# Kernel tuning notes

Hardware: AMD Instinct MI355X
Metric: run time of the kernel (lower is better)

Reference implementation:

```python
import jax, jax.numpy as jnp
from jax import lax
import numpy as np

B, NUM_TPM, NUM_CNV, NODE_DIM, DRUG_FEAT = 32, 16000, 16000, 36, 75
N_DRUGS, N_ATOMS, N_PAIRS = 128, 64, 4096


def setup_inputs() -> dict:
    key = jax.random.key(0)
    ks = jax.random.split(key, 32)

    def w(k, shape):
        fan_in = shape[0] if len(shape) == 2 else int(np.prod(shape[1:]))
        return (jax.random.normal(k, shape, jnp.float32) / np.float32(np.sqrt(fan_in))).astype(jnp.float32)

    pic_dim = jax.random.normal(ks[0], (B, 3, 256, 256), jnp.float32)
    rna_seq = jax.random.normal(ks[1], (B, NUM_TPM), jnp.float32)
    gene_cnv = jax.random.normal(ks[2], (B, NUM_CNV), jnp.float32)
    drug_fea = jax.random.uniform(ks[3], (N_DRUGS, N_ATOMS, DRUG_FEAT), jnp.float32)
    a = (jax.random.uniform(ks[4], (N_DRUGS, N_ATOMS, N_ATOMS)) < 0.15).astype(jnp.float32)
    drug_adj = jnp.maximum(a, jnp.transpose(a, (0, 2, 1)))
    index_list = jnp.stack([
        jax.random.randint(ks[5], (N_PAIRS,), 0, B),
        jax.random.randint(ks[6], (N_PAIRS,), 0, N_DRUGS)], axis=1)
    target = jax.random.randint(ks[7], (N_PAIRS,), 0, 2)
    logit_scale = jnp.asarray(10.0, jnp.float32)
    return dict(
        pic_dim=pic_dim, rna_seq=rna_seq, gene_cnv=gene_cnv,
        drug_fea=drug_fea, drug_adj=drug_adj, index_list=index_list,
        target=target, logit_scale=logit_scale,
        conv_w=w(ks[8], (32, 3, 5, 5)), conv_b=jnp.zeros((32,), jnp.float32),
        fc1_w=w(ks[9], (32 * 128 * 128, 1024)), fc1_b=jnp.zeros((1024,), jnp.float32),
        fc2_w=w(ks[10], (1024, 36)), fc2_b=jnp.zeros((36,), jnp.float32),
        mlp1_w1=w(ks[11], (NUM_TPM, NUM_TPM // 4)), mlp1_b1=jnp.zeros((NUM_TPM // 4,), jnp.float32),
        mlp1_w2=w(ks[12], (NUM_TPM // 4, NODE_DIM)), mlp1_b2=jnp.zeros((NODE_DIM,), jnp.float32),
        mlp2_w1=w(ks[13], (NUM_CNV, NUM_CNV // 4)), mlp2_b1=jnp.zeros((NUM_CNV // 4,), jnp.float32),
        mlp2_w2=w(ks[14], (NUM_CNV // 4, NODE_DIM)), mlp2_b2=jnp.zeros((NODE_DIM,), jnp.float32),
        att_w1=w(ks[15], (36, 128)), att_b1=jnp.zeros((128,), jnp.float32),
        att_w2=w(ks[16], (128, 1)),
        end_w1=w(ks[17], (NODE_DIM * 4, NODE_DIM)), end_b1=jnp.zeros((NODE_DIM,), jnp.float32),
        end_w2=w(ks[18], (NODE_DIM, 2)), end_b2=jnp.zeros((2,), jnp.float32),
        gcn_w=w(ks[19], (DRUG_FEAT, NODE_DIM * 8)), gcn_w2=w(ks[20], (NODE_DIM * 8, NODE_DIM * 2)))


def _mlp(x, w1, b1, w2, b2):  # Linear-ReLU-(Dropout eval)-Linear-Softmax
    h = jax.nn.relu(x @ w1 + b1)
    return jax.nn.softmax(h @ w2 + b2, axis=-1)


def _ce(logits, labels):  # mean cross entropy, labels int [N]
    lp = jax.nn.log_softmax(logits, axis=-1)
    return -jnp.take_along_axis(lp, labels[:, None], axis=1).mean()


def reference(pic_dim, rna_seq, gene_cnv, drug_fea, drug_adj, index_list, target,
              logit_scale, conv_w, conv_b, fc1_w, fc1_b, fc2_w, fc2_b,
              mlp1_w1, mlp1_b1, mlp1_w2, mlp1_b2, mlp2_w1, mlp2_b1, mlp2_w2, mlp2_b2,
              att_w1, att_b1, att_w2, end_w1, end_b1, end_w2, end_b2, gcn_w, gcn_w2):
    # omics branches
    rna1 = _mlp(rna_seq, mlp1_w1, mlp1_b1, mlp1_w2, mlp1_b2)    # [B,36]
    cnv1 = _mlp(gene_cnv, mlp2_w1, mlp2_b1, mlp2_w2, mlp2_b2)   # [B,36]
    # image branch: conv(3->32,k5,p2) + relu + maxpool2 + fc
    x = lax.conv_general_dilated(pic_dim, conv_w, (1, 1), [(2, 2), (2, 2)])
    x = jax.nn.relu(x + conv_b[None, :, None, None])
    x = lax.reduce_window(x, -jnp.inf, lax.max, (1, 1, 2, 2), (1, 1, 2, 2), 'VALID')
    x = x.reshape(x.shape[0], -1)                               # [B, 32*128*128]
    x = jax.nn.relu(x @ fc1_w + fc1_b)
    pic1 = x @ fc2_w + fc2_b                                    # [B,36]
    # semantic attention over the two omics views
    z = jnp.stack([rna1, cnv1], axis=1)                         # [B,2,36]
    wv = (jnp.tanh(z @ att_w1 + att_b1) @ att_w2).mean(0)       # [2,1]
    beta = jax.nn.softmax(wv, axis=0)
    cell = (beta[None] * z).sum(1)                              # [B,36]
    # CLIP-style loss
    pic1 = pic1 / jnp.linalg.norm(pic1, axis=1, keepdims=True)
    cell = cell / jnp.linalg.norm(cell, axis=1, keepdims=True)
    image_fea = logit_scale * (pic1 @ cell.T)
    labels = jnp.arange(image_fea.shape[0])
    total_loss2 = (_ce(image_fea, labels) + _ce(image_fea.T, labels)) / 2
    cell_cat = jnp.concatenate([cell, pic1], axis=1)            # [B,72]
    # batched drug GCN (replaces per-drug python loop)
    eye = jnp.eye(N_ATOMS, dtype=jnp.float32)
    def gcn_one(X, A):
        Ht = A.T * (1.0 - eye) + eye        # set diagonal to 1 (add self loops)
        deg = Ht.sum(1)
        dinv = jnp.where(deg == 0, 0.0, 1.0 / deg)
        Hn = dinv[:, None] * Ht             # D^-1 A_hat  (== H.t() after norm)
        out = Hn @ ((Hn @ (X @ gcn_w)) @ gcn_w2)
        return jnp.max(jax.nn.relu(out), axis=0)  # max over atoms -> [72]
    drugfea = jax.vmap(gcn_one)(drug_fea, drug_adj)             # [n_drugs,72]
    # pair prediction head
    Bc = jnp.concatenate([cell_cat[index_list[:, 0]], drugfea[index_list[:, 1]]], axis=1)
    Bp = _mlp(Bc, end_w1, end_b1, end_w2, end_b2)               # [n_pairs,2]
    loss1 = _ce(Bp, target)
    return (loss1, total_loss2, Bp, target)
```

## Files before the change

### kernel.cpp

```cpp
#include <hip/hip_runtime.h>
#include <hip/hip_bf16.h>
#include <math.h>

typedef float evf4 __attribute__((ext_vector_type(4)));

__device__ __forceinline__ void fma4(float4& a, float s, const float4& v) {
  a.x += s * v.x; a.y += s * v.y; a.z += s * v.z; a.w += s * v.w;
}
__device__ __forceinline__ float4 ntload4(const float4* p) {
  evf4 v = __builtin_nontemporal_load((const evf4*)p);
  return make_float4(v.x, v.y, v.z, v.w);
}
__device__ __forceinline__ float ntload1(const float* p) {
  return __builtin_nontemporal_load(p);
}

__device__ __forceinline__ void conv_body(
    const float* __restrict__ pic, const float* __restrict__ cw,
    const float* __restrict__ cb, float* __restrict__ pooled,
    int bid, float tile[3][8][260]) {
  int php = bid & 63, ocg2 = (bid >> 6) & 1, b = bid >> 7;
  int tid = threadIdx.x;
  int pw = tid & 127, phl = tid >> 7;
  int ph = php * 2 + phl;
  int h_base = php * 4 - 2;
  for (int i = tid; i < 3 * 8 * 260; i += 256) {
    int c = i % 260; int rr = (i / 260) & 7; int ic = i / (260 * 8);
    int h = h_base + rr, w = c - 2;
    float v = 0.f;
    if (h >= 0 && h < 256 && w >= 0 && w < 256)
      v = pic[((size_t)b * 3 + ic) * 65536 + h * 256 + w];
    tile[ic][rr][c] = v;
  }
  __syncthreads();
  float acc[16][4];
#pragma unroll
  for (int o = 0; o < 16; ++o)
#pragma unroll
    for (int q = 0; q < 4; ++q) acc[o][q] = 0.f;
  int r0 = phl * 2;
  int c0 = pw * 2;
#pragma unroll
  for (int ic = 0; ic < 3; ++ic) {
    float win[6][6];
#pragma unroll
    for (int r = 0; r < 6; ++r)
#pragma unroll
      for (int cc = 0; cc < 6; ++cc) win[r][cc] = tile[ic][r0 + r][c0 + cc];
#pragma unroll
    for (int o = 0; o < 16; ++o) {
      const float* __restrict__ wk = cw + ((ocg2 * 16 + o) * 3 + ic) * 25;
#pragma unroll
      for (int kh = 0; kh < 5; ++kh)
#pragma unroll
        for (int kw = 0; kw < 5; ++kw) {
          float wv = wk[kh * 5 + kw];
          acc[o][0] += win[kh][kw] * wv;
          acc[o][1] += win[kh][kw + 1] * wv;
          acc[o][2] += win[kh + 1][kw] * wv;
          acc[o][3] += win[kh + 1][kw + 1] * wv;
        }
    }
  }
#pragma unroll
  for (int o = 0; o < 16; ++o) {
    float m = fmaxf(fmaxf(acc[o][0], acc[o][1]), fmaxf(acc[o][2], acc[o][3]));
    m = fmaxf(m + cb[ocg2 * 16 + o], 0.f);
    pooled[(((size_t)b * 32 + ocg2 * 16 + o) * 128 + ph) * 128 + pw] = m;
  }
}

__device__ __forceinline__ void wc_body(
    const float* __restrict__ w1, const float* __restrict__ w2,
    float* __restrict__ wc, int bx) {
  int i = bx * 256 + threadIdx.x;
  if (i >= 75 * 72) return;
  int r = i / 72, c = i - r * 72;
  float s = 0.f;
  for (int k = 0; k < 288; ++k) s += w1[r * 288 + k] * w2[k * 72 + c];
  wc[i] = s;
}

__global__ __launch_bounds__(256) void k1_conv_wc_kernel(
    const float* __restrict__ pic, const float* __restrict__ cw,
    const float* __restrict__ cb, float* __restrict__ pooled,
    const float* __restrict__ gw, const float* __restrict__ gw2,
    float* __restrict__ wcb) {
  __shared__ float tile[3][8][260];
  int bid = blockIdx.x;
  if (bid < 4096) conv_body(pic, cw, cb, pooled, bid, tile);
  else            wc_body(gw, gw2, wcb, bid - 4096);
}

__device__ __forceinline__ void gemm32p_body(
    const float* __restrict__ X, const float* __restrict__ W,
    float* __restrict__ partial, int K, int N, int chunk,
    int bx, int split, float xs[128][36]) {
  int tid = threadIdx.x;
  int colv = bx * 256 + tid;
  int col0 = colv * 4;
  bool active = col0 < N;
  int k0 = split * chunk, k1 = min(k0 + chunk, K);
  size_t Nv = (size_t)(N >> 2);
  const float4* Wv = (const float4*)W;
  float4 acc[32];
#pragma unroll
  for (int b = 0; b < 32; ++b) acc[b] = make_float4(0.f, 0.f, 0.f, 0.f);

  float4 xpre[4];
#pragma unroll
  for (int j = 0; j < 4; ++j) {
    int idx = tid + j * 256;
    int b = idx >> 5, kk = (idx & 31) * 4;
    xpre[j] = *(const float4*)&X[(size_t)b * K + k0 + kk];
  }

  auto fmablk = [&](int kk, const float4& w4) {
    const float4* xr = (const float4*)xs[kk];
#pragma unroll
    for (int b4 = 0; b4 < 8; ++b4) {
      float4 xv = xr[b4];
      fma4(acc[b4 * 4 + 0], xv.x, w4);
      fma4(acc[b4 * 4 + 1], xv.y, w4);
      fma4(acc[b4 * 4 + 2], xv.z, w4);
      fma4(acc[b4 * 4 + 3], xv.w, w4);
    }
  };

  for (int kt = k0; kt < k1; kt += 128) {
    __syncthreads();
#pragma unroll
    for (int j = 0; j < 4; ++j) {
      int idx = tid + j * 256;
      int b = idx >> 5, kk = (idx & 31) * 4;
      xs[kk + 0][b] = xpre[j].x;
      xs[kk + 1][b] = xpre[j].y;
      xs[kk + 2][b] = xpre[j].z;
      xs[kk + 3][b] = xpre[j].w;
    }
    __syncthreads();
    if (kt + 128 < k1) {
#pragma unroll
      for (int j = 0; j < 4; ++j) {
        int idx = tid + j * 256;
        int b = idx >> 5, kk = (idx & 31) * 4;
        xpre[j] = *(const float4*)&X[(size_t)b * K + kt + 128 + kk];
      }
    }
    if (active) {
      const float4* wp = Wv + (size_t)kt * Nv + colv;
      float4 cur[8], nxt[8];
#pragma unroll
      for (int j = 0; j < 8; ++j) cur[j] = ntload4(wp + (size_t)j * Nv);
#pragma unroll 1
      for (int g = 0; g < 15; ++g) {
        const float4* wn = wp + 8 * Nv;
#pragma unroll
        for (int j = 0; j < 8; ++j) nxt[j] = ntload4(wn + (size_t)j * Nv);
        int kb = g * 8;
#pragma unroll
        for (int j = 0; j < 8; ++j) fmablk(kb + j, cur[j]);
#pragma unroll
        for (int j = 0; j < 8; ++j) cur[j] = nxt[j];
        wp = wn;
      }
#pragma unroll
      for (int j = 0; j < 8; ++j) fmablk(120 + j, cur[j]);
    }
  }
  if (active) {
    float* p = partial + (size_t)split * 32 * N + col0;
#pragma unroll
    for (int b = 0; b < 32; ++b) *(float4*)(p + (size_t)b * N) = acc[b];
  }
}

__global__ __launch_bounds__(256) void gemm_all_kernel(
    const float* __restrict__ pooled, const float* __restrict__ fc1w,
    float* __restrict__ pfc1,
    const float* __restrict__ rna, const float* __restrict__ m1w1, float* __restrict__ pm1,
    const float* __restrict__ cnv, const float* __restrict__ m2w1, float* __restrict__ pm2) {
  __shared__ float xs[128][36];
  int b = blockIdx.x;
  if (b < 512) {
    gemm32p_body(pooled, fc1w, pfc1, 524288, 1024, 1024, 0, b, xs);
  } else {
    int j = b - 512;
    int z = j / 252;
    int r = j % 252;
    int bx = r & 3, split = r >> 2;
    if (z == 0) gemm32p_body(rna, m1w1, pm1, 16000, 4000, 256, bx, split, xs);
    else        gemm32p_body(cnv, m2w1, pm2, 16000, 4000, 256, bx, split, xs);
  }
}

__device__ __forceinline__ void reduce_s1_body(
    const float* __restrict__ partial, float* __restrict__ p2, int N,
    int bx, int sy) {
  int i = bx * 256 + threadIdx.x;
  if (i >= 32 * N) return;
  const float* p = partial + (size_t)(sy * 128) * 32 * N + i;
  size_t st = (size_t)32 * N;
  float s0 = 0, s1 = 0, s2 = 0, s3 = 0, s4 = 0, s5 = 0, s6 = 0, s7 = 0;
  for (int sp = 0; sp < 128; sp += 8) {
    s0 += ntload1(p + (sp + 0) * st); s1 += ntload1(p + (sp + 1) * st);
    s2 += ntload1(p + (sp + 2) * st); s3 += ntload1(p + (sp + 3) * st);
    s4 += ntload1(p + (sp + 4) * st); s5 += ntload1(p + (sp + 5) * st);
    s6 += ntload1(p + (sp + 6) * st); s7 += ntload1(p + (sp + 7) * st);
  }
  p2[(size_t)sy * 32 * N + i] = ((s0 + s1) + (s2 + s3)) + ((s4 + s5) + (s6 + s7));
}

__device__ __forceinline__ void reduce8_body(
    const float* __restrict__ partial, const float* __restrict__ bias,
    float* __restrict__ out, int N, int nsplit, int relu, int bx) {
  int i = bx * 256 + threadIdx.x;
  if (i >= 32 * N) return;
  int col = i % N;
  const float* p = partial + i;
  size_t st = (size_t)32 * N;
  float s0 = 0, s1 = 0, s2 = 0, s3 = 0, s4 = 0, s5 = 0, s6 = 0, s7 = 0;
  int sp = 0;
  for (; sp + 8 <= nsplit; sp += 8) {
    s0 += ntload1(p + (sp + 0) * st); s1 += ntload1(p + (sp + 1) * st);
    s2 += ntload1(p + (sp + 2) * st); s3 += ntload1(p + (sp + 3) * st);
    s4 += ntload1(p + (sp + 4) * st); s5 += ntload1(p + (sp + 5) * st);
    s6 += ntload1(p + (sp + 6) * st); s7 += ntload1(p + (sp + 7) * st);
  }
  for (; sp < nsplit; ++sp) s0 += ntload1(p + (size_t)sp * st);
  float s = bias[col] + (((s0 + s1) + (s2 + s3)) + ((s4 + s5) + (s6 + s7)));
  out[i] = relu ? fmaxf(s, 0.f) : s;
}

__global__ __launch_bounds__(256) void k3_reduce_kernel(
    const float* __restrict__ pfc1, float* __restrict__ p2fc1,
    const float* __restrict__ pm1, const float* __restrict__ m1b1, float* __restrict__ h1,
    const float* __restrict__ pm2, const float* __restrict__ m2b1, float* __restrict__ h2) {
  int b = blockIdx.x;
  if (b < 512) {
    reduce_s1_body(pfc1, p2fc1, 1024, b & 127, b >> 7);
  } else {
    int idx = b - 512;
    if (idx < 500) reduce8_body(pm1, m1b1, h1, 4000, 63, 1, idx);
    else           reduce8_body(pm2, m2b1, h2, 4000, 63, 1, idx - 500);
  }
}

__device__ __forceinline__ void reduce_s2_body(
    const float* __restrict__ p2, const float* __restrict__ bias,
    float* __restrict__ out, int N, int nsy, int relu, int bx) {
  int i = bx * 256 + threadIdx.x;
  if (i >= 32 * N) return;
  int col = i % N;
  float s = bias[col];
  for (int sy = 0; sy < nsy; ++sy) s += p2[(size_t)sy * 32 * N + i];
  out[i] = relu ? fmaxf(s, 0.f) : s;
}

__device__ __forceinline__ void gcn_body(
    const float* __restrict__ Xg, const float* __restrict__ Ag,
    const float* __restrict__ Wc, float* __restrict__ drugfea, int d,
    float Hn[64][65], float Xs[64][75], float Wcs[75][72],
    float Ys[64][72], float Ts[64][72]) {
  int tid = threadIdx.x;
  const float* Ad = Ag + (size_t)d * 4096;
  const float* Xd = Xg + (size_t)d * 4800;
  for (int i = tid; i < 4096; i += 256) {
    int r = i & 63, c = i >> 6;
    Hn[r][c] = (r == c) ? 1.f : Ad[c * 64 + r];
  }
  for (int i = tid; i < 4800; i += 256) Xs[i / 75][i % 75] = Xd[i];
  for (int i = tid; i < 5400; i += 256) Wcs[i / 72][i % 72] = Wc[i];
  __syncthreads();
  if (tid < 64) {
    float s = 0.f;
    for (int c = 0; c < 64; ++c) s += Hn[tid][c];
    float inv = (s == 0.f) ? 0.f : 1.f / s;
    for (int c = 0; c < 64; ++c) Hn[tid][c] *= inv;
  }
  __syncthreads();
  int rb = tid >> 3, cb = tid & 7;
  int r0 = rb * 2, c0 = cb * 9;
  {
    float o0[9], o1[9];
#pragma unroll
    for (int j = 0; j < 9; ++j) { o0[j] = 0.f; o1[j] = 0.f; }
    for (int k = 0; k < 75; ++k) {
      float x0 = Xs[r0][k], x1 = Xs[r0 + 1][k];
#pragma unroll
      for (int j = 0; j < 9; ++j) {
        float w = Wcs[k][c0 + j];
        o0[j] += x0 * w; o1[j] += x1 * w;
      }
    }
#pragma unroll
    for (int j = 0; j < 9; ++j) { Ys[r0][c0 + j] = o0[j]; Ys[r0 + 1][c0 + j] = o1[j]; }
  }
  __syncthreads();
  {
    float o0[9], o1[9];
#pragma unroll
    for (int j = 0; j < 9; ++j) { o0[j] = 0.f; o1[j] = 0.f; }
    for (int k = 0; k < 64; ++k) {
      float x0 = Hn[r0][k], x1 = Hn[r0 + 1][k];
#pragma unroll
      for (int j = 0; j < 9; ++j) {
        float w = Ys[k][c0 + j];
        o0[j] += x0 * w; o1[j] += x1 * w;
      }
    }
#pragma unroll
    for (int j = 0; j < 9; ++j) { Ts[r0][c0 + j] = o0[j]; Ts[r0 + 1][c0 + j] = o1[j]; }
  }
  __syncthreads();
  {
    float o0[9], o1[9];
#pragma unroll
    for (int j = 0; j < 9; ++j) { o0[j] = 0.f; o1[j] = 0.f; }
    for (int k = 0; k < 64; ++k) {
      float x0 = Hn[r0][k], x1 = Hn[r0 + 1][k];
#pragma unroll
      for (int j = 0; j < 9; ++j) {
        float w = Ts[k][c0 + j];
        o0[j] += x0 * w; o1[j] += x1 * w;
      }
    }
#pragma unroll
    for (int j = 0; j < 9; ++j) {
      Ys[r0][c0 + j] = fmaxf(o0[j], 0.f);
      Ys[r0 + 1][c0 + j] = fmaxf(o1[j], 0.f);
    }
  }
  __syncthreads();
  if (tid < 72) {
    float m = Ys[0][tid];
    for (int i = 1; i < 64; ++i) m = fmaxf(m, Ys[i][tid]);
    drugfea[d * 72 + tid] = m;
  }
}

__global__ __launch_bounds__(256) void k4_s2_gcn_kernel(
    const float* __restrict__ p2fc1, const float* __restrict__ fc1_b,
    float* __restrict__ fcact,
    const float* __restrict__ Xg, const float* __restrict__ Ag,
    const float* __restrict__ wcb, float* __restrict__ drugfea) {
  __shared__ float Hn[64][65];
  __shared__ float Xs[64][75];
  __shared__ float Wcs[75][72];
  __shared__ float Ys[64][72];
  __shared__ float Ts[64][72];
  int b = blockIdx.x;
  if (b < 128) reduce_s2_body(p2fc1, fc1_b, fcact, 1024, 4, 1, b);
  else         gcn_body(Xg, Ag, wcb, drugfea, b - 128, Hn, Xs, Wcs, Ys, Ts);
}

__global__ __launch_bounds__(256) void lin36_all_kernel(
    const float* __restrict__ X0, const float* __restrict__ W0,
    const float* __restrict__ bi0, float* __restrict__ out0,
    const float* __restrict__ X1, const float* __restrict__ W1,
    const float* __restrict__ bi1, float* __restrict__ out1,
    const float* __restrict__ X2, const float* __restrict__ W2,
    const float* __restrict__ bi2, float* __restrict__ out2) {
  const float* X; const float* W; const float* bias; float* out; int K; bool do_sm;
  if (blockIdx.y == 0)      { X = X0; W = W0; bias = bi0; out = out0; K = 4000; do_sm = true; }
  else if (blockIdx.y == 1) { X = X1; W = W1; bias = bi1; out = out1; K = 4000; do_sm = true; }
  else                      { X = X2; W = W2; bias = bi2; out = out2; K = 1024; do_sm = false; }
  __shared__ float xs[4000];
  __shared__ float red[28][36];
  __shared__ float vals[36];
  __shared__ float mxv, smv;
  int b = blockIdx.x, tid = threadIdx.x;
  for (int i = tid; i < K; i += 256) xs[i] = X[(size_t)b * K + i];
  __syncthreads();
  if (tid < 252) {
    int c4 = tid % 9, g = tid / 9;
    const float4* W4 = (const float4*)W;
    float4 s = make_float4(0.f, 0.f, 0.f, 0.f);
    for (int k = g; k < K; k += 28) fma4(s, xs[k], W4[k * 9 + c4]);
    red[g][c4 * 4 + 0] = s.x; red[g][c4 * 4 + 1] = s.y;
    red[g][c4 * 4 + 2] = s.z; red[g][c4 * 4 + 3] = s.w;
  }
  __syncthreads();
  if (tid < 36) {
    float s = bias[tid];
    for (int g = 0; g < 28; ++g) s += red[g][tid];
    vals[tid] = s;
  }
  __syncthreads();
  if (do_sm) {
    if (tid == 0) {
      float m = -1e30f;
      for (int j = 0; j < 36; ++j) m = fmaxf(m, vals[j]);
      float e = 0.f;
      for (int j = 0; j < 36; ++j) e += expf(vals[j] - m);
      mxv = m; smv = e;
    }
    __syncthreads();
    if (tid < 36) out[b * 36 + tid] = expf(vals[tid] - mxv) / smv;
  } else {
    if (tid < 36) out[b * 36 + tid] = vals[tid];
  }
}

__global__ __launch_bounds__(256) void head_kernel(
    const float* __restrict__ rna1, const float* __restrict__ cnv1,
    const float* __restrict__ pic1r, const float* __restrict__ aw1,
    const float* __restrict__ ab1, const float* __restrict__ aw2,
    const float* __restrict__ scale_p, float* __restrict__ cell_cat,
    float* __restrict__ dout) {
  __shared__ float z[2][32][36];
  __shared__ float pic1n[32][36];
  __shared__ float celln[32][36];
  __shared__ float fea[32][32];
  __shared__ float wvp[64];
  __shared__ float beta0, beta1;
  __shared__ float rowl[32], coll[32];
  int tid = threadIdx.x;
  for (int i = tid; i < 1152; i += 256) {
    int b = i / 36, k = i - (i / 36) * 36;
    z[0][b][k] = rna1[i];
    z[1][b][k] = cnv1[i];
    pic1n[b][k] = pic1r[i];
  }
  __syncthreads();
  {
    int p = tid >> 2, sub = tid & 3;
    int b = p >> 1, v = p & 1;
    float s = 0.f;
    for (int h = sub; h < 128; h += 4) {
      float a = ab1[h];
      for (int k = 0; k < 36; ++k) a += z[v][b][k] * aw1[k * 128 + h];
      s += tanhf(a) * aw2[h];
    }
    s += __shfl_down(s, 1, 64);
    s += __shfl_down(s, 2, 64);
    if (sub == 0) wvp[p] = s;
  }
  __syncthreads();
  if (tid == 0) {
    float w0 = 0.f, w1 = 0.f;
    for (int b = 0; b < 32; ++b) { w0 += wvp[b * 2]; w1 += wvp[b * 2 + 1]; }
    w0 /= 32.f; w1 /= 32.f;
    float m = fmaxf(w0, w1);
    float e0 = expf(w0 - m), e1 = expf(w1 - m);
    beta0 = e0 / (e0 + e1); beta1 = e1 / (e0 + e1);
  }
  __syncthreads();
  for (int i = tid; i < 1152; i += 256) {
    int b = i / 36, k = i - (i / 36) * 36;
    celln[b][k] = beta0 * z[0][b][k] + beta1 * z[1][b][k];
  }
  __syncthreads();
  if (tid < 32) {
    float s = 0.f;
    for (int k = 0; k < 36; ++k) { float x = pic1n[tid][k]; s += x * x; }
    float inv = 1.f / sqrtf(s);
    for (int k = 0; k < 36; ++k) pic1n[tid][k] *= inv;
  } else if (tid < 64) {
    int b = tid - 32;
    float s = 0.f;
    for (int k = 0; k < 36; ++k) { float x = celln[b][k]; s += x * x; }
    float inv = 1.f / sqrtf(s);
    for (int k = 0; k < 36; ++k) celln[b][k] *= inv;
  }
  __syncthreads();
  for (int i = tid; i < 1152; i += 256) {
    int b = i / 36, k = i - (i / 36) * 36;
    cell_cat[b * 72 + k] = celln[b][k];
    cell_cat[b * 72 + 36 + k] = pic1n[b][k];
  }
  float sc = *scale_p;
  for (int t = tid; t < 1024; t += 256) {
    int i = t >> 5, j = t & 31;
    float s = 0.f;
    for (int k = 0; k < 36; ++k) s += pic1n[i][k] * celln[j][k];
    fea[i][j] = sc * s;
  }
  __syncthreads();
  if (tid < 32) {
    float m = -1e30f;
    for (int j = 0; j < 32; ++j) m = fmaxf(m, fea[tid][j]);
    float e = 0.f;
    for (int j = 0; j < 32; ++j) e += expf(fea[tid][j] - m);
    rowl[tid] = (logf(e) + m) - fea[tid][tid];
  } else if (tid < 64) {
    int j = tid - 32;
    float m = -1e30f;
    for (int i = 0; i < 32; ++i) m = fmaxf(m, fea[i][j]);
    float e = 0.f;
    for (int i = 0; i < 32; ++i) e += expf(fea[i][j] - m);
    coll[j] = (logf(e) + m) - fea[j][j];
  }
  __syncthreads();
  if (tid == 0) {
    float s1 = 0.f, s2 = 0.f;
    for (int i = 0; i < 32; ++i) { s1 += rowl[i]; s2 += coll[i]; }
    dout[1] = 0.5f * (s1 / 32.f + s2 / 32.f);
  }
}

__global__ __launch_bounds__(256) void pair_kernel(
    const float* __restrict__ cell_cat, const float* __restrict__ drugfea,
    const int* __restrict__ idx, const int* __restrict__ target,
    const float* __restrict__ w1, const float* __restrict__ b1,
    const float* __restrict__ w2, const float* __restrict__ b2,
    float* __restrict__ bp_out, float* __restrict__ tgt_out,
    float* __restrict__ blocksums) {
  __shared__ float w1s[144][36];
  __shared__ float ccs[32][73];
  __shared__ float dfs[128][73];
  __shared__ float w2s[72], b2s[2];
  __shared__ float lsum[256];
  int tid = threadIdx.x;
  {
    float4* dst = (float4*)&w1s[0][0];
    const float4* src = (const float4*)w1;
    for (int i = tid; i < 1296; i += 256) dst[i] = src[i];
  }
  for (int i = tid; i < 2304; i += 256) ccs[i / 72][i % 72] = cell_cat[i];
  for (int i = tid; i < 9216; i += 256) dfs[i / 72][i % 72] = drugfea[i];
  if (tid < 72) w2s[tid] = w2[tid];
  if (tid < 2) b2s[tid] = b2[tid];
  __syncthreads();
  int p = blockIdx.x * 256 + tid;
  int ci = idx[p * 2], dj = idx[p * 2 + 1];
  float4 h4[9];
  {
    const float4* bb = (const float4*)b1;
#pragma unroll
    for (int q = 0; q < 9; ++q) h4[q] = bb[q];
  }
  for (int k = 0; k < 72; ++k) {
    float x = ccs[ci][k];
    const float4* wr = (const float4*)&w1s[k][0];
#pragma unroll
    for (int q = 0; q < 9; ++q) fma4(h4[q], x, wr[q]);
  }
  for (int k = 0; k < 72; ++k) {
    float x = dfs[dj][k];
    const float4* wr = (const float4*)&w1s[72 + k][0];
#pragma unroll
    for (int q = 0; q < 9; ++q) fma4(h4[q], x, wr[q]);
  }
  float l0 = b2s[0], l1 = b2s[1];
#pragma unroll
  for (int q = 0; q < 9; ++q) {
    float hv;
    hv = fmaxf(h4[q].x, 0.f); l0 += hv * w2s[(q * 4 + 0) * 2]; l1 += hv * w2s[(q * 4 + 0) * 2 + 1];
    hv = fmaxf(h4[q].y, 0.f); l0 += hv * w2s[(q * 4 + 1) * 2]; l1 += hv * w2s[(q * 4 + 1) * 2 + 1];
    hv = fmaxf(h4[q].z, 0.f); l0 += hv * w2s[(q * 4 + 2) * 2]; l1 += hv * w2s[(q * 4 + 2) * 2 + 1];
    hv = fmaxf(h4[q].w, 0.f); l0 += hv * w2s[(q * 4 + 3) * 2]; l1 += hv * w2s[(q * 4 + 3) * 2 + 1];
  }
  float m = fmaxf(l0, l1);
  float e0 = expf(l0 - m), e1 = expf(l1 - m);
  float inv = 1.f / (e0 + e1);
  float p0 = e0 * inv, p1 = e1 * inv;
  bp_out[p * 2] = p0;
  bp_out[p * 2 + 1] = p1;
  int t = target[p];
  float mm = fmaxf(p0, p1);
  float lse = logf(expf(p0 - mm) + expf(p1 - mm)) + mm;
  float chosen = t ? p1 : p0;
  lsum[tid] = lse - chosen;
  tgt_out[p] = (float)t;
  __syncthreads();
  for (int s = 128; s > 0; s >>= 1) {
    if (tid < s) lsum[tid] += lsum[tid + s];
    __syncthreads();
  }
  if (tid == 0) blocksums[blockIdx.x] = lsum[0];
}

__global__ void final_kernel(const float* __restrict__ blocksums, float* __restrict__ dout) {
  if (threadIdx.x == 0 && blockIdx.x == 0) {
    float s = 0.f;
    for (int i = 0; i < 16; ++i) s += blocksums[i];
    dout[0] = s / 4096.f;
  }
}

extern "C" void kernel_launch(void* const* d_in, const int* in_sizes, int n_in,
                              void* d_out, int out_size, void* d_ws, size_t ws_size,
                              hipStream_t stream) {
  (void)in_sizes; (void)n_in; (void)out_size; (void)ws_size;
  const float* pic        = (const float*)d_in[0];
  const float* rna        = (const float*)d_in[1];
  const float* cnv        = (const float*)d_in[2];
  const float* drug_fea   = (const float*)d_in[3];
  const float* drug_adj   = (const float*)d_in[4];
  const int*   index_list = (const int*)d_in[5];
  const int*   target     = (const int*)d_in[6];
  const float* logit_scale= (const float*)d_in[7];
  const float* conv_w     = (const float*)d_in[8];
  const float* conv_b     = (const float*)d_in[9];
  const float* fc1_w      = (const float*)d_in[10];
  const float* fc1_b      = (const float*)d_in[11];
  const float* fc2_w      = (const float*)d_in[12];
  const float* fc2_b      = (const float*)d_in[13];
  const float* m1w1       = (const float*)d_in[14];
  const float* m1b1       = (const float*)d_in[15];
  const float* m1w2       = (const float*)d_in[16];
  const float* m1b2       = (const float*)d_in[17];
  const float* m2w1       = (const float*)d_in[18];
  const float* m2b1       = (const float*)d_in[19];
  const float* m2w2       = (const float*)d_in[20];
  const float* m2b2       = (const float*)d_in[21];
  const float* aw1        = (const float*)d_in[22];
  const float* ab1        = (const float*)d_in[23];
  const float* aw2        = (const float*)d_in[24];
  const float* ew1        = (const float*)d_in[25];
  const float* eb1        = (const float*)d_in[26];
  const float* ew2        = (const float*)d_in[27];
  const float* eb2        = (const float*)d_in[28];
  const float* gw         = (const float*)d_in[29];
  const float* gw2        = (const float*)d_in[30];

  float* ws = (float*)d_ws;
  float* pooled  = ws;
  float* pfc1    = ws + 16777216;
  float* p2fc1   = ws + 33554432;
  float* pm1     = ws + 33685504;
  float* pm2     = ws + 41749504;
  float* fcact   = ws + 49813504;
  float* h1      = ws + 49846272;
  float* h2      = ws + 49974272;
  float* rna1    = ws + 50102272;
  float* cnv1    = ws + 50103424;
  float* pic1r   = ws + 50104576;
  float* wcb     = ws + 50105728;
  float* drugf   = ws + 50111128;
  float* cellcat = ws + 50120344;
  float* bsums   = ws + 50122648;

  float* out = (float*)d_out;

  k1_conv_wc_kernel<<<4118, 256, 0, stream>>>(pic, conv_w, conv_b, pooled,
                                              gw, gw2, wcb);
  gemm_all_kernel<<<1016, 256, 0, stream>>>(pooled, fc1_w, pfc1,
                                            rna, m1w1, pm1, cnv, m2w1, pm2);
  k3_reduce_kernel<<<1512, 256, 0, stream>>>(pfc1, p2fc1,
                                             pm1, m1b1, h1, pm2, m2b1, h2);
  k4_s2_gcn_kernel<<<256, 256, 0, stream>>>(p2fc1, fc1_b, fcact,
                                            drug_fea, drug_adj, wcb, drugf);
  {
    dim3 g(32, 3);
    lin36_all_kernel<<<g, 256, 0, stream>>>(h1, m1w2, m1b2, rna1,
                                            h2, m2w2, m2b2, cnv1,
                                            fcact, fc2_w, fc2_b, pic1r);
  }
  head_kernel<<<1, 256, 0, stream>>>(rna1, cnv1, pic1r, aw1, ab1, aw2,
                                     logit_scale, cellcat, out);
  pair_kernel<<<16, 256, 0, stream>>>(cellcat, drugf, index_list, target,
                                      ew1, eb1, ew2, eb2,
                                      out + 2, out + 2 + 8192, bsums);
  final_kernel<<<1, 64, 0, stream>>>(bsums, out);
}
```

Before: 1.007 ms.

## Narrow GEMM columns per thread to two and vectorize split-K reductions

The split-K GEMM body now handles two output columns per thread instead of four. This halves the accumulator registers so the kernel can declare four blocks per SIMD, and the grid grows to cover the same work (fc1 now uses 256 splits of 2048 with two column blocks). The register prefetch of the X tile for the next step is dropped. The reduction kernels are rewritten to use float4 nontemporal loads with hardcoded sizes, so fewer blocks are launched. The trade-off is less reuse of each shared-memory X read per weight load, and the X load latency is no longer hidden behind the compute.

After: 1.993 ms. 97.9% more time.

```diff
diff --git a/kernel.cpp b/kernel.cpp
--- a/kernel.cpp
+++ b/kernel.cpp
@@ -3,6 +3,7 @@
 #include <math.h>
 
 typedef float evf4 __attribute__((ext_vector_type(4)));
+typedef float evf2 __attribute__((ext_vector_type(2)));
 
 __device__ __forceinline__ void fma4(float4& a, float s, const float4& v) {
   a.x += s * v.x; a.y += s * v.y; a.z += s * v.z; a.w += s * v.w;
@@ -11,8 +12,9 @@
   evf4 v = __builtin_nontemporal_load((const evf4*)p);
   return make_float4(v.x, v.y, v.z, v.w);
 }
-__device__ __forceinline__ float ntload1(const float* p) {
-  return __builtin_nontemporal_load(p);
+__device__ __forceinline__ float2 ntload2(const float2* p) {
+  evf2 v = __builtin_nontemporal_load((const evf2*)p);
+  return make_float2(v.x, v.y);
 }
 
 __device__ __forceinline__ void conv_body(
@@ -92,38 +94,30 @@
   else            wc_body(gw, gw2, wcb, bid - 4096);
 }
 
-__device__ __forceinline__ void gemm32p_body(
+__device__ __forceinline__ void gemm2c_body(
     const float* __restrict__ X, const float* __restrict__ W,
     float* __restrict__ partial, int K, int N, int chunk,
     int bx, int split, float xs[128][36]) {
   int tid = threadIdx.x;
   int colv = bx * 256 + tid;
-  int col0 = colv * 4;
+  int col0 = colv * 2;
   bool active = col0 < N;
   int k0 = split * chunk, k1 = min(k0 + chunk, K);
-  size_t Nv = (size_t)(N >> 2);
-  const float4* Wv = (const float4*)W;
-  float4 acc[32];
-#pragma unroll
-  for (int b = 0; b < 32; ++b) acc[b] = make_float4(0.f, 0.f, 0.f, 0.f);
-
-  float4 xpre[4];
-#pragma unroll
-  for (int j = 0; j < 4; ++j) {
-    int idx = tid + j * 256;
-    int b = idx >> 5, kk = (idx & 31) * 4;
-    xpre[j] = *(const float4*)&X[(size_t)b * K + k0 + kk];
-  }
-
-  auto fmablk = [&](int kk, const float4& w4) {
+  size_t Nv = (size_t)(N >> 1);
+  const float2* Wv = (const float2*)W;
+  float2 acc[32];
+#pragma unroll
+  for (int b = 0; b < 32; ++b) acc[b] = make_float2(0.f, 0.f);
+
+  auto fmablk = [&](int kk, const float2& w2) {
     const float4* xr = (const float4*)xs[kk];
 #pragma unroll
     for (int b4 = 0; b4 < 8; ++b4) {
       float4 xv = xr[b4];
-      fma4(acc[b4 * 4 + 0], xv.x, w4);
-      fma4(acc[b4 * 4 + 1], xv.y, w4);
-      fma4(acc[b4 * 4 + 2], xv.z, w4);
-      fma4(acc[b4 * 4 + 3], xv.w, w4);
+      acc[b4 * 4 + 0].x += xv.x * w2.x; acc[b4 * 4 + 0].y += xv.x * w2.y;
+      acc[b4 * 4 + 1].x += xv.y * w2.x; acc[b4 * 4 + 1].y += xv.y * w2.y;
+      acc[b4 * 4 + 2].x += xv.z * w2.x; acc[b4 * 4 + 2].y += xv.z * w2.y;
+      acc[b4 * 4 + 3].x += xv.w * w2.x; acc[b4 * 4 + 3].y += xv.w * w2.y;
     }
   };
 
@@ -133,30 +127,21 @@
     for (int j = 0; j < 4; ++j) {
       int idx = tid + j * 256;
       int b = idx >> 5, kk = (idx & 31) * 4;
-      xs[kk + 0][b] = xpre[j].x;
-      xs[kk + 1][b] = xpre[j].y;
-      xs[kk + 2][b] = xpre[j].z;
-      xs[kk + 3][b] = xpre[j].w;
+      float4 x = *(const float4*)&X[(size_t)b * K + kt + kk];
+      xs[kk + 0][b] = x.x; xs[kk + 1][b] = x.y;
+      xs[kk + 2][b] = x.z; xs[kk + 3][b] = x.w;
     }
     __syncthreads();
-    if (kt + 128 < k1) {
-#pragma unroll
-      for (int j = 0; j < 4; ++j) {
-        int idx = tid + j * 256;
-        int b = idx >> 5, kk = (idx & 31) * 4;
-        xpre[j] = *(const float4*)&X[(size_t)b * K + kt + 128 + kk];
-      }
-    }
     if (active) {
-      const float4* wp = Wv + (size_t)kt * Nv + colv;
-      float4 cur[8], nxt[8];
-#pragma unroll
-      for (int j = 0; j < 8; ++j) cur[j] = ntload4(wp + (size_t)j * Nv);
+      const float2* wp = Wv + (size_t)kt * Nv + colv;
+      float2 cur[8], nxt[8];
+#pragma unroll
+      for (int j = 0; j < 8; ++j) cur[j] = ntload2(wp + (size_t)j * Nv);
 #pragma unroll 1
       for (int g = 0; g < 15; ++g) {
-        const float4* wn = wp + 8 * Nv;
-#pragma unroll
-        for (int j = 0; j < 8; ++j) nxt[j] = ntload4(wn + (size_t)j * Nv);
+        const float2* wn = wp + 8 * Nv;
+#pragma unroll
+        for (int j = 0; j < 8; ++j) nxt[j] = ntload2(wn + (size_t)j * Nv);
         int kb = g * 8;
 #pragma unroll
         for (int j = 0; j < 8; ++j) fmablk(kb + j, cur[j]);
@@ -171,11 +156,11 @@
   if (active) {
     float* p = partial + (size_t)split * 32 * N + col0;
 #pragma unroll
-    for (int b = 0; b < 32; ++b) *(float4*)(p + (size_t)b * N) = acc[b];
-  }
-}
-
-__global__ __launch_bounds__(256) void gemm_all_kernel(
+    for (int b = 0; b < 32; ++b) *(float2*)(p + (size_t)b * N) = acc[b];
+  }
+}
+
+__global__ __launch_bounds__(256, 4) void gemm_all_kernel(
     const float* __restrict__ pooled, const float* __restrict__ fc1w,
     float* __restrict__ pfc1,
     const float* __restrict__ rna, const float* __restrict__ m1w1, float* __restrict__ pm1,
@@ -183,53 +168,65 @@
   __shared__ float xs[128][36];
   int b = blockIdx.x;
   if (b < 512) {
-    gemm32p_body(pooled, fc1w, pfc1, 524288, 1024, 1024, 0, b, xs);
+    gemm2c_body(pooled, fc1w, pfc1, 524288, 1024, 2048, b & 1, b >> 1, xs);
   } else {
     int j = b - 512;
-    int z = j / 252;
-    int r = j % 252;
-    int bx = r & 3, split = r >> 2;
-    if (z == 0) gemm32p_body(rna, m1w1, pm1, 16000, 4000, 256, bx, split, xs);
-    else        gemm32p_body(cnv, m2w1, pm2, 16000, 4000, 256, bx, split, xs);
-  }
+    int z = j / 504;
+    int r = j % 504;
+    int bx = r & 7, split = r >> 3;
+    if (z == 0) gemm2c_body(rna, m1w1, pm1, 16000, 4000, 256, bx, split, xs);
+    else        gemm2c_body(cnv, m2w1, pm2, 16000, 4000, 256, bx, split, xs);
+  }
+}
+
+__device__ __forceinline__ void fadd4(float4& a, const float4& v) {
+  a.x += v.x; a.y += v.y; a.z += v.z; a.w += v.w;
 }
 
 __device__ __forceinline__ void reduce_s1_body(
-    const float* __restrict__ partial, float* __restrict__ p2, int N,
+    const float* __restrict__ partial, float* __restrict__ p2,
     int bx, int sy) {
   int i = bx * 256 + threadIdx.x;
-  if (i >= 32 * N) return;
-  const float* p = partial + (size_t)(sy * 128) * 32 * N + i;
-  size_t st = (size_t)32 * N;
-  float s0 = 0, s1 = 0, s2 = 0, s3 = 0, s4 = 0, s5 = 0, s6 = 0, s7 = 0;
-  for (int sp = 0; sp < 128; sp += 8) {
-    s0 += ntload1(p + (sp + 0) * st); s1 += ntload1(p + (sp + 1) * st);
-    s2 += ntload1(p + (sp + 2) * st); s3 += ntload1(p + (sp + 3) * st);
-    s4 += ntload1(p + (sp + 4) * st); s5 += ntload1(p + (sp + 5) * st);
-    s6 += ntload1(p + (sp + 6) * st); s7 += ntload1(p + (sp + 7) * st);
-  }
-  p2[(size_t)sy * 32 * N + i] = ((s0 + s1) + (s2 + s3)) + ((s4 + s5) + (s6 + s7));
-}
-
-__device__ __forceinline__ void reduce8_body(
+  const float4* p = (const float4*)partial + (size_t)(sy * 128) * 8192 + i;
+  const size_t st = 8192;
+  float4 s0 = make_float4(0, 0, 0, 0), s1 = s0, s2 = s0, s3 = s0;
+  for (int sp = 0; sp < 128; sp += 4) {
+    fadd4(s0, ntload4(p + (sp + 0) * st));
+    fadd4(s1, ntload4(p + (sp + 1) * st));
+    fadd4(s2, ntload4(p + (sp + 2) * st));
+    fadd4(s3, ntload4(p + (sp + 3) * st));
+  }
+  float4 r;
+  r.x = (s0.x + s1.x) + (s2.x + s3.x);
+  r.y = (s0.y + s1.y) + (s2.y + s3.y);
+  r.z = (s0.z + s1.z) + (s2.z + s3.z);
+  r.w = (s0.w + s1.w) + (s2.w + s3.w);
+  ((float4*)p2)[(size_t)sy * 8192 + i] = r;
+}
+
+__device__ __forceinline__ void reduce_mlp_body(
     const float* __restrict__ partial, const float* __restrict__ bias,
-    float* __restrict__ out, int N, int nsplit, int relu, int bx) {
+    float* __restrict__ out, int bx) {
   int i = bx * 256 + threadIdx.x;
-  if (i >= 32 * N) return;
-  int col = i % N;
-  const float* p = partial + i;
-  size_t st = (size_t)32 * N;
-  float s0 = 0, s1 = 0, s2 = 0, s3 = 0, s4 = 0, s5 = 0, s6 = 0, s7 = 0;
+  if (i >= 32000) return;
+  const float4* p = (const float4*)partial + i;
+  const size_t st = 32000;
+  float4 s0 = make_float4(0, 0, 0, 0), s1 = s0, s2 = s0, s3 = s0;
   int sp = 0;
-  for (; sp + 8 <= nsplit; sp += 8) {
-    s0 += ntload1(p + (sp + 0) * st); s1 += ntload1(p + (sp + 1) * st);
-    s2 += ntload1(p + (sp + 2) * st); s3 += ntload1(p + (sp + 3) * st);
-    s4 += ntload1(p + (sp + 4) * st); s5 += ntload1(p + (sp + 5) * st);
-    s6 += ntload1(p + (sp + 6) * st); s7 += ntload1(p + (sp + 7) * st);
-  }
-  for (; sp < nsplit; ++sp) s0 += ntload1(p + (size_t)sp * st);
-  float s = bias[col] + (((s0 + s1) + (s2 + s3)) + ((s4 + s5) + (s6 + s7)));
-  out[i] = relu ? fmaxf(s, 0.f) : s;
+  for (; sp + 4 <= 63; sp += 4) {
+    fadd4(s0, ntload4(p + (sp + 0) * st));
+    fadd4(s1, ntload4(p + (sp + 1) * st));
+    fadd4(s2, ntload4(p + (sp + 2) * st));
+    fadd4(s3, ntload4(p + (sp + 3) * st));
+  }
+  for (; sp < 63; ++sp) fadd4(s0, ntload4(p + (size_t)sp * st));
+  float4 bi = ((const float4*)bias)[i % 1000];
+  float4 r;
+  r.x = fmaxf(bi.x + (s0.x + s1.x) + (s2.x + s3.x), 0.f);
+  r.y = fmaxf(bi.y + (s0.y + s1.y) + (s2.y + s3.y), 0.f);
+  r.z = fmaxf(bi.z + (s0.z + s1.z) + (s2.z + s3.z), 0.f);
+  r.w = fmaxf(bi.w + (s0.w + s1.w) + (s2.w + s3.w), 0.f);
+  ((float4*)out)[i] = r;
 }
 
 __global__ __launch_bounds__(256) void k3_reduce_kernel(
@@ -237,24 +234,28 @@
     const float* __restrict__ pm1, const float* __restrict__ m1b1, float* __restrict__ h1,
     const float* __restrict__ pm2, const float* __restrict__ m2b1, float* __restrict__ h2) {
   int b = blockIdx.x;
-  if (b < 512) {
-    reduce_s1_body(pfc1, p2fc1, 1024, b & 127, b >> 7);
+  if (b < 64) {
+    reduce_s1_body(pfc1, p2fc1, b & 31, b >> 5);
   } else {
-    int idx = b - 512;
-    if (idx < 500) reduce8_body(pm1, m1b1, h1, 4000, 63, 1, idx);
-    else           reduce8_body(pm2, m2b1, h2, 4000, 63, 1, idx - 500);
+    int idx = b - 64;
+    if (idx < 125) reduce_mlp_body(pm1, m1b1, h1, idx);
+    else           reduce_mlp_body(pm2, m2b1, h2, idx - 125);
   }
 }
 
 __device__ __forceinline__ void reduce_s2_body(
     const float* __restrict__ p2, const float* __restrict__ bias,
-    float* __restrict__ out, int N, int nsy, int relu, int bx) {
+    float* __restrict__ out, int bx) {
   int i = bx * 256 + threadIdx.x;
-  if (i >= 32 * N) return;
-  int col = i % N;
-  float s = bias[col];
-  for (int sy = 0; sy < nsy; ++sy) s += p2[(size_t)sy * 32 * N + i];
-  out[i] = relu ? fmaxf(s, 0.f) : s;
+  float4 a = ((const float4*)p2)[i];
+  float4 b = ((const float4*)p2)[8192 + i];
+  float4 bi = ((const float4*)bias)[i & 255];
+  float4 r;
+  r.x = fmaxf(bi.x + a.x + b.x, 0.f);
+  r.y = fmaxf(bi.y + a.y + b.y, 0.f);
+  r.z = fmaxf(bi.z + a.z + b.z, 0.f);
+  r.w = fmaxf(bi.w + a.w + b.w, 0.f);
+  ((float4*)out)[i] = r;
 }
 
 __device__ __forceinline__ void gcn_body(
@@ -350,8 +351,8 @@
   __shared__ float Ys[64][72];
   __shared__ float Ts[64][72];
   int b = blockIdx.x;
-  if (b < 128) reduce_s2_body(p2fc1, fc1_b, fcact, 1024, 4, 1, b);
-  else         gcn_body(Xg, Ag, wcb, drugfea, b - 128, Hn, Xs, Wcs, Ys, Ts);
+  if (b < 32) reduce_s2_body(p2fc1, fc1_b, fcact, b);
+  else        gcn_body(Xg, Ag, wcb, drugfea, b - 32, Hn, Xs, Wcs, Ys, Ts);
 }
 
 __global__ __launch_bounds__(256) void lin36_all_kernel(
@@ -636,11 +637,11 @@
 
   k1_conv_wc_kernel<<<4118, 256, 0, stream>>>(pic, conv_w, conv_b, pooled,
                                               gw, gw2, wcb);
-  gemm_all_kernel<<<1016, 256, 0, stream>>>(pooled, fc1_w, pfc1,
+  gemm_all_kernel<<<1520, 256, 0, stream>>>(pooled, fc1_w, pfc1,
                                             rna, m1w1, pm1, cnv, m2w1, pm2);
-  k3_reduce_kernel<<<1512, 256, 0, stream>>>(pfc1, p2fc1,
-                                             pm1, m1b1, h1, pm2, m2b1, h2);
-  k4_s2_gcn_kernel<<<256, 256, 0, stream>>>(p2fc1, fc1_b, fcact,
+  k3_reduce_kernel<<<314, 256, 0, stream>>>(pfc1, p2fc1,
+                                            pm1, m1b1, h1, pm2, m2b1, h2);
+  k4_s2_gcn_kernel<<<160, 256, 0, stream>>>(p2fc1, fc1_b, fcact,
                                             drug_fea, drug_adj, wcb, drugf);
   {
     dim3 g(32, 3);
```
